# Kernel optimization log

Hardware: AMD Instinct MI355X
Metric: run time of the kernel (lower is better)

## Reference

```python
import jax, jax.numpy as jnp
import numpy as np

B, N, C = 64, 1700, 256
E_SP, E_TM = 6400, 10000


def gcn_conv(x, W, b, edge_index, num_nodes):
    """PyG GCNConv (normalize=True, add_self_loops=True) on batched [B,N,C] input,
    gathering/scattering along the node axis (node_dim=-2)."""
    row, col = edge_index[0], edge_index[1]
    loops = jnp.arange(num_nodes, dtype=row.dtype)
    row = jnp.concatenate([row, loops])
    col = jnp.concatenate([col, loops])
    w = jnp.ones(row.shape[0], dtype=x.dtype)
    deg = jax.ops.segment_sum(w, col, num_segments=num_nodes)
    dinv = jnp.where(deg > 0, jax.lax.rsqrt(deg), jnp.zeros_like(deg))
    norm = dinv[row] * dinv[col]                      # [E+N]
    h = x @ W                                         # [B,N,Cout]
    msg = h[:, row, :] * norm[None, :, None]          # gather along joints
    out = jnp.zeros((x.shape[0], num_nodes, W.shape[1]), x.dtype)
    out = out.at[:, col, :].add(msg)                  # scatter-add along joints
    return out + b


def setup_inputs() -> dict:
    key = jax.random.key(0)
    ks = jax.random.split(key, 9)
    s = 1.0 / np.sqrt(C)
    return {
        "x": jax.random.normal(ks[0], (B, N, C), jnp.float32),
        "W1": jax.random.uniform(ks[1], (C, C), jnp.float32, -s, s),
        "b1": jnp.zeros((C,), jnp.float32),
        "W2": jax.random.uniform(ks[2], (C, C), jnp.float32, -s, s),
        "b2": jnp.zeros((C,), jnp.float32),
        "W3": jax.random.uniform(ks[3], (C, C), jnp.float32, -s, s),
        "b3": jnp.zeros((C,), jnp.float32),
        "keypoint_line_without_temporal": jax.random.randint(ks[4], (2, E_SP), 0, N, jnp.int32),
        "keypoint_line_with_temporal": jax.random.randint(ks[5], (2, E_TM), 0, N, jnp.int32),
    }


def reference(x, W1, b1, W2, b2, W3, b3,
              keypoint_line_without_temporal, keypoint_line_with_temporal):
    num_nodes = x.shape[1]
    residual = x  # downsample is None -> identity residual
    out = jax.nn.relu(gcn_conv(x, W1, b1, keypoint_line_without_temporal, num_nodes))
    out = jax.nn.relu(gcn_conv(out, W2, b2, keypoint_line_with_temporal, num_nodes))
    out = gcn_conv(out, W3, b3, keypoint_line_without_temporal, num_nodes)
    return jax.nn.relu(out + residual)
```

## Files before the change

### kernel.cpp

```cpp
#include <hip/hip_runtime.h>

#define NNODES 1700
#define CDIM   256

typedef __attribute__((ext_vector_type(8))) short bf16x8;
typedef __attribute__((ext_vector_type(4))) float f32x4;

__device__ inline float bf2f(unsigned h) { return __uint_as_float(h << 16); }
__device__ inline unsigned short f2bf(float f) {
  unsigned u = __float_as_uint(f);
  u = (u + 0x7FFFu + ((u >> 16) & 1u)) >> 16;
  return (unsigned short)u;
}

__device__ inline void async_copy16(const void* gsrc, void* ldst) {
  __builtin_amdgcn_global_load_lds(
      (const __attribute__((address_space(1))) unsigned int*)gsrc,
      (__attribute__((address_space(3))) unsigned int*)ldst,
      16, 0, 0);
}


__global__ __launch_bounds__(256) void prep1(const float* __restrict__ W1,
                                             const float* __restrict__ W2,
                                             const float* __restrict__ W3,
                                             unsigned short* __restrict__ Wt,
                                             int* __restrict__ zb) {
  int i = blockIdx.x * 256 + threadIdx.x;
  if (i < 4 * NNODES) zb[i] = 0;
  if (i < 3 * 65536) {
    int wsel = i >> 16, e = i & 65535;
    const float* W = wsel == 0 ? W1 : (wsel == 1 ? W2 : W3);
    int k = e >> 8, n = e & 255;
    Wt[(wsel << 16) + n * 256 + k] = f2bf(W[e]);
  }
}

__global__ __launch_bounds__(256) void prep2(const int* __restrict__ esp, int Esp,
                                             const int* __restrict__ etm, int Etm,
                                             int* __restrict__ cnt_sp,
                                             int* __restrict__ cnt_tm) {
  int i = blockIdx.x * 256 + threadIdx.x;
  if (i < Esp) {
    atomicAdd(&cnt_sp[esp[Esp + i]], 1);
  } else {
    int k = i - Esp;
    if (k < Etm) atomicAdd(&cnt_tm[etm[Etm + k]], 1);
  }
}

__global__ __launch_bounds__(1024) void prep3(const int* __restrict__ cnt_sp,
                                              float* __restrict__ dinv_sp,
                                              int* __restrict__ off_sp,
                                              const int* __restrict__ cnt_tm,
                                              float* __restrict__ dinv_tm,
                                              int* __restrict__ off_tm) {
  const int* cnt = blockIdx.x ? cnt_tm : cnt_sp;
  float* dinv = blockIdx.x ? dinv_tm : dinv_sp;
  int* off = blockIdx.x ? off_tm : off_sp;
  __shared__ int s[2048];
  int t = threadIdx.x;
  for (int i = t; i < NNODES; i += 1024) dinv[i] = rsqrtf((float)(cnt[i] + 1));
  for (int i = t; i < 2048; i += 1024) s[i] = (i < NNODES) ? (cnt[i] + 1) : 0;
  for (int d = 1; d < 2048; d <<= 1) {
    __syncthreads();
    int idx = (t + 1) * (d << 1) - 1;
    if (idx < 2048) s[idx] += s[idx - d];
  }
  __syncthreads();
  if (t == 0) s[2047] = 0;
  for (int d = 1024; d >= 1; d >>= 1) {
    __syncthreads();
    int idx = (t + 1) * (d << 1) - 1;
    if (idx < 2048) { int tmp = s[idx - d]; s[idx - d] = s[idx]; s[idx] += tmp; }
  }
  __syncthreads();
  for (int i = t; i <= NNODES; i += 1024) off[i] = s[i];
}

__global__ __launch_bounds__(256) void prep4(
    const int* __restrict__ esp, int Esp, const int* __restrict__ etm, int Etm,
    const float* __restrict__ dinv_sp, const int* __restrict__ off_sp,
    int* __restrict__ cur_sp, int* __restrict__ src_sp, float* __restrict__ wgt_sp,
    const float* __restrict__ dinv_tm, const int* __restrict__ off_tm,
    int* __restrict__ cur_tm, int* __restrict__ src_tm, float* __restrict__ wgt_tm) {
  int i = blockIdx.x * 256 + threadIdx.x;
  const int tot_sp = Esp + NNODES;
  if (i < tot_sp) {
    int s, d;
    if (i < Esp) { s = esp[i]; d = esp[Esp + i]; } else { s = d = i - Esp; }
    float w = dinv_sp[s] * dinv_sp[d];
    int p = atomicAdd(&cur_sp[d], 1);
    int idx = off_sp[d] + p;
    src_sp[idx] = s; wgt_sp[idx] = w;
  } else {
    int k = i - tot_sp;
    if (k < Etm + NNODES) {
      int s, d;
      if (k < Etm) { s = etm[k]; d = etm[Etm + k]; } else { s = d = k - Etm; }
      float w = dinv_tm[s] * dinv_tm[d];
      int p = atomicAdd(&cur_tm[d], 1);
      int idx = off_tm[d] + p;
      src_tm[idx] = s; wgt_tm[idx] = w;
    }
  }
}


template <bool SRCF32>
__global__ __launch_bounds__(256) void agg_kernel(const void* __restrict__ Xp,
                                                  const int* __restrict__ off,
                                                  const int* __restrict__ srcv,
                                                  const float* __restrict__ wv,
                                                  unsigned short* __restrict__ Xa) {
  const int n = blockIdx.x;
  const int b = blockIdx.y * 8 + (threadIdx.x >> 5);
  const int c = (threadIdx.x & 31) * 8;
  const int beg = off[n], end = off[n + 1];
  const size_t base = (size_t)b * NNODES;

  float a0 = 0.f, a1 = 0.f, a2 = 0.f, a3 = 0.f;
  float a4 = 0.f, a5 = 0.f, a6 = 0.f, a7 = 0.f;
  for (int i = beg; i < end; i += 2) {
    int s0 = srcv[i];
    float w0 = wv[i];
    const bool two = (i + 1 < end);
    int i1 = two ? i + 1 : i;
    int s1 = srcv[i1];
    float w1 = two ? wv[i1] : 0.f;
    if (SRCF32) {
      const float* X = (const float*)Xp;
      const float* p0 = X + (base + s0) * CDIM + c;
      const float* p1 = X + (base + s1) * CDIM + c;
      float4 u0 = *(const float4*)p0, u1 = *(const float4*)(p0 + 4);
      float4 v0 = *(const float4*)p1, v1 = *(const float4*)(p1 + 4);
      a0 += w0 * u0.x + w1 * v0.x; a1 += w0 * u0.y + w1 * v0.y;
      a2 += w0 * u0.z + w1 * v0.z; a3 += w0 * u0.w + w1 * v0.w;
      a4 += w0 * u1.x + w1 * v1.x; a5 += w0 * u1.y + w1 * v1.y;
      a6 += w0 * u1.z + w1 * v1.z; a7 += w0 * u1.w + w1 * v1.w;
    } else {
      const unsigned short* X = (const unsigned short*)Xp;
      uint4 u = *(const uint4*)(X + (base + s0) * CDIM + c);
      uint4 v = *(const uint4*)(X + (base + s1) * CDIM + c);
      a0 += w0 * bf2f(u.x & 0xffffu) + w1 * bf2f(v.x & 0xffffu);
      a1 += w0 * bf2f(u.x >> 16)     + w1 * bf2f(v.x >> 16);
      a2 += w0 * bf2f(u.y & 0xffffu) + w1 * bf2f(v.y & 0xffffu);
      a3 += w0 * bf2f(u.y >> 16)     + w1 * bf2f(v.y >> 16);
      a4 += w0 * bf2f(u.z & 0xffffu) + w1 * bf2f(v.z & 0xffffu);
      a5 += w0 * bf2f(u.z >> 16)     + w1 * bf2f(v.z >> 16);
      a6 += w0 * bf2f(u.w & 0xffffu) + w1 * bf2f(v.w & 0xffffu);
      a7 += w0 * bf2f(u.w >> 16)     + w1 * bf2f(v.w >> 16);
    }
  }
  bf16x8 ov;
  ov[0] = (short)f2bf(a0); ov[1] = (short)f2bf(a1);
  ov[2] = (short)f2bf(a2); ov[3] = (short)f2bf(a3);
  ov[4] = (short)f2bf(a4); ov[5] = (short)f2bf(a5);
  ov[6] = (short)f2bf(a6); ov[7] = (short)f2bf(a7);
  *(bf16x8*)(Xa + (base + n) * CDIM + c) = ov;
}


template <int K>
__device__ __forceinline__ void kstep(const unsigned short* __restrict__ asrc,
                                      const unsigned short* __restrict__ bsrc,
                                      unsigned short (&As)[3][128 * 32],
                                      unsigned short (&Bs)[3][256 * 32],
                                      int t, int wm, int wn, int lr, int lk,
                                      f32x4 (&acc)[4][4]) {
  if constexpr (K < 7) {
    asm volatile("s_waitcnt vmcnt(3)" ::: "memory");
  } else {
    asm volatile("s_waitcnt vmcnt(0)" ::: "memory");
  }
  __builtin_amdgcn_s_barrier();
  if constexpr (K + 2 < 8) {
    constexpr int S = K + 2;
    async_copy16(asrc + S * 32, &As[S % 3][t * 8]);
    async_copy16(bsrc + S * 32, &Bs[S % 3][t * 8]);
    async_copy16(bsrc + 128 * CDIM + S * 32, &Bs[S % 3][4096 + t * 8]);
  }
  bf16x8 a[4], b[4];
#pragma unroll
  for (int i = 0; i < 4; i++)
    a[i] = *(const bf16x8*)&As[K % 3][(wm + i * 16 + lr) * 32 + lk];
#pragma unroll
  for (int i = 0; i < 4; i++)
    b[i] = *(const bf16x8*)&Bs[K % 3][(wn + i * 16 + lr) * 32 + lk];
#pragma unroll
  for (int mi = 0; mi < 4; mi++)
#pragma unroll
    for (int ni = 0; ni < 4; ni++)
      acc[mi][ni] = __builtin_amdgcn_mfma_f32_16x16x32_bf16(a[mi], b[ni], acc[mi][ni], 0, 0, 0);
}

template <bool FINAL>
__global__ __launch_bounds__(512, 4) void gemm_n256(const unsigned short* __restrict__ A,
                                                    const unsigned short* __restrict__ Wt,
                                                    const float* __restrict__ bias,
                                                    const float* __restrict__ resid,
                                                    void* __restrict__ outp) {
  __shared__ __align__(16) unsigned short As[3][128 * 32];
  __shared__ __align__(16) unsigned short Bs[3][256 * 32];
  const int m0 = blockIdx.x * 128;
  const int t = threadIdx.x;
  const int lane = t & 63;
  const int w = t >> 6;
  const int wm = (w & 1) * 64;
  const int wn = (w >> 1) * 64;
  const int lr = lane & 15;
  const int lk = (lane >> 4) * 8;

  const unsigned short* asrc = A + (size_t)(m0 + (t >> 2)) * CDIM + (t & 3) * 8;
  const unsigned short* bsrc = Wt + (size_t)(t >> 2) * CDIM + (t & 3) * 8;

  f32x4 acc[4][4] = {};

#pragma unroll
  for (int s = 0; s < 2; s++) {
    async_copy16(asrc + s * 32, &As[s][t * 8]);
    async_copy16(bsrc + s * 32, &Bs[s][t * 8]);
    async_copy16(bsrc + 128 * CDIM + s * 32, &Bs[s][4096 + t * 8]);
  }

  kstep<0>(asrc, bsrc, As, Bs, t, wm, wn, lr, lk, acc);
  kstep<1>(asrc, bsrc, As, Bs, t, wm, wn, lr, lk, acc);
  kstep<2>(asrc, bsrc, As, Bs, t, wm, wn, lr, lk, acc);
  kstep<3>(asrc, bsrc, As, Bs, t, wm, wn, lr, lk, acc);
  kstep<4>(asrc, bsrc, As, Bs, t, wm, wn, lr, lk, acc);
  kstep<5>(asrc, bsrc, As, Bs, t, wm, wn, lr, lk, acc);
  kstep<6>(asrc, bsrc, As, Bs, t, wm, wn, lr, lk, acc);
  kstep<7>(asrc, bsrc, As, Bs, t, wm, wn, lr, lk, acc);

  float bv[4];
#pragma unroll
  for (int ni = 0; ni < 4; ni++) bv[ni] = bias[wn + ni * 16 + lr];
  const int orow = (lane >> 4) * 4;
#pragma unroll
  for (int mi = 0; mi < 4; mi++) {
#pragma unroll
    for (int ni = 0; ni < 4; ni++) {
#pragma unroll
      for (int r = 0; r < 4; r++) {
        const size_t gr = (size_t)(m0 + wm + mi * 16 + orow + r);
        const size_t idx = gr * CDIM + wn + ni * 16 + lr;
        float v = acc[mi][ni][r] + bv[ni];
        if (FINAL) {
          v += resid[idx];
          ((float*)outp)[idx] = fmaxf(v, 0.f);
        } else {
          ((unsigned short*)outp)[idx] = f2bf(fmaxf(v, 0.f));
        }
      }
    }
  }
}


extern "C" void kernel_launch(void* const* d_in, const int* in_sizes, int n_in,
                              void* d_out, int out_size, void* d_ws, size_t ws_size,
                              hipStream_t stream) {
  const float* x  = (const float*)d_in[0];
  const float* W1 = (const float*)d_in[1];
  const float* b1 = (const float*)d_in[2];
  const float* W2 = (const float*)d_in[3];
  const float* b2 = (const float*)d_in[4];
  const float* W3 = (const float*)d_in[5];
  const float* b3 = (const float*)d_in[6];
  const int* esp = (const int*)d_in[7];
  const int* etm = (const int*)d_in[8];

  const int Esp = in_sizes[7] / 2;
  const int Etm = in_sizes[8] / 2;
  const int B = in_sizes[0] / (NNODES * CDIM);
  const int M = B * NNODES;

  char* ws = (char*)d_ws;
  size_t woff = 0;
  auto alloc = [&](size_t bytes) -> void* {
    void* p = ws + woff;
    woff = (woff + bytes + 255) & ~(size_t)255;
    return p;
  };

  unsigned short* H   = (unsigned short*)alloc((size_t)M * CDIM * 2);
  unsigned short* Act = (unsigned short*)alloc((size_t)M * CDIM * 2);
  unsigned short* Wt  = (unsigned short*)alloc((size_t)3 * CDIM * CDIM * 2);
  int* zero_base = (int*)alloc((size_t)4 * NNODES * sizeof(int));
  int* cnt_sp = zero_base;
  int* cur_sp = zero_base + NNODES;
  int* cnt_tm = zero_base + 2 * NNODES;
  int* cur_tm = zero_base + 3 * NNODES;
  int* off_sp = (int*)alloc((NNODES + 1) * sizeof(int));
  int* off_tm = (int*)alloc((NNODES + 1) * sizeof(int));
  float* dinv_sp = (float*)alloc(NNODES * sizeof(float));
  float* dinv_tm = (float*)alloc(NNODES * sizeof(float));
  int*   src_sp = (int*)alloc((size_t)(Esp + NNODES) * sizeof(int));
  float* wgt_sp = (float*)alloc((size_t)(Esp + NNODES) * sizeof(float));
  int*   src_tm = (int*)alloc((size_t)(Etm + NNODES) * sizeof(int));
  float* wgt_tm = (float*)alloc((size_t)(Etm + NNODES) * sizeof(float));

  prep1<<<(3 * 65536 + 255) / 256, 256, 0, stream>>>(W1, W2, W3, Wt, zero_base);
  prep2<<<(Esp + Etm + 255) / 256, 256, 0, stream>>>(esp, Esp, etm, Etm, cnt_sp, cnt_tm);
  prep3<<<2, 1024, 0, stream>>>(cnt_sp, dinv_sp, off_sp, cnt_tm, dinv_tm, off_tm);
  prep4<<<(Esp + Etm + 2 * NNODES + 255) / 256, 256, 0, stream>>>(
      esp, Esp, etm, Etm, dinv_sp, off_sp, cur_sp, src_sp, wgt_sp,
      dinv_tm, off_tm, cur_tm, src_tm, wgt_tm);

  dim3 agrid(NNODES, B / 8);
  dim3 ggrid(M / 128);

  agg_kernel<true><<<agrid, 256, 0, stream>>>(x, off_sp, src_sp, wgt_sp, Act);
  gemm_n256<false><<<ggrid, 512, 0, stream>>>(Act, Wt, b1, nullptr, H);
  agg_kernel<false><<<agrid, 256, 0, stream>>>(H, off_tm, src_tm, wgt_tm, Act);
  gemm_n256<false><<<ggrid, 512, 0, stream>>>(Act, Wt + CDIM * CDIM, b2, nullptr, H);
  agg_kernel<false><<<agrid, 256, 0, stream>>>(H, off_sp, src_sp, wgt_sp, Act);
  gemm_n256<true><<<ggrid, 512, 0, stream>>>(Act, Wt + 2 * CDIM * CDIM, b3, x, d_out);
}
```

Before: 465.9 us.

## Split GEMM into 128x64 tiles with swizzled block order and double buffering

The GEMM no longer computes one 128x256 output tile per 512-thread block. It now launches four times as many 256-thread blocks, each producing a 128x64 tile. Blocks are remapped with a chunked swizzle so neighbouring blocks share A rows in cache. The LDS pipeline drops from a triple buffer to a double buffer, with an extra barrier after fragment reads so the next prefetch can safely overwrite the buffer. The goal is more blocks for occupancy and load balance on the 256 CUs, at the cost of reading each A tile four times and adding a barrier per k-step.

```diff
diff --git a/kernel.cpp b/kernel.cpp
--- a/kernel.cpp
+++ b/kernel.cpp
@@ -164,63 +164,70 @@
 template <int K>
 __device__ __forceinline__ void kstep(const unsigned short* __restrict__ asrc,
                                       const unsigned short* __restrict__ bsrc,
-                                      unsigned short (&As)[3][128 * 32],
-                                      unsigned short (&Bs)[3][256 * 32],
+                                      unsigned short (&As)[2][128 * 32],
+                                      unsigned short (&Bs)[2][64 * 32],
                                       int t, int wm, int wn, int lr, int lk,
-                                      f32x4 (&acc)[4][4]) {
+                                      f32x4 (&acc)[4][2]) {
   if constexpr (K < 7) {
     asm volatile("s_waitcnt vmcnt(3)" ::: "memory");
   } else {
     asm volatile("s_waitcnt vmcnt(0)" ::: "memory");
   }
   __builtin_amdgcn_s_barrier();
+  bf16x8 a[4], b[2];
+#pragma unroll
+  for (int i = 0; i < 4; i++)
+    a[i] = *(const bf16x8*)&As[K & 1][(wm + i * 16 + lr) * 32 + lk];
+#pragma unroll
+  for (int i = 0; i < 2; i++)
+    b[i] = *(const bf16x8*)&Bs[K & 1][(wn + i * 16 + lr) * 32 + lk];
+  asm volatile("s_waitcnt lgkmcnt(0)" ::: "memory");
+  __builtin_amdgcn_sched_barrier(0);
+  __builtin_amdgcn_s_barrier();
   if constexpr (K + 2 < 8) {
     constexpr int S = K + 2;
-    async_copy16(asrc + S * 32, &As[S % 3][t * 8]);
-    async_copy16(bsrc + S * 32, &Bs[S % 3][t * 8]);
-    async_copy16(bsrc + 128 * CDIM + S * 32, &Bs[S % 3][4096 + t * 8]);
-  }
-  bf16x8 a[4], b[4];
-#pragma unroll
-  for (int i = 0; i < 4; i++)
-    a[i] = *(const bf16x8*)&As[K % 3][(wm + i * 16 + lr) * 32 + lk];
-#pragma unroll
-  for (int i = 0; i < 4; i++)
-    b[i] = *(const bf16x8*)&Bs[K % 3][(wn + i * 16 + lr) * 32 + lk];
+    async_copy16(asrc + S * 32, &As[S & 1][t * 8]);
+    async_copy16(asrc + (size_t)64 * CDIM + S * 32, &As[S & 1][2048 + t * 8]);
+    async_copy16(bsrc + S * 32, &Bs[S & 1][t * 8]);
+  }
 #pragma unroll
   for (int mi = 0; mi < 4; mi++)
 #pragma unroll
-    for (int ni = 0; ni < 4; ni++)
+    for (int ni = 0; ni < 2; ni++)
       acc[mi][ni] = __builtin_amdgcn_mfma_f32_16x16x32_bf16(a[mi], b[ni], acc[mi][ni], 0, 0, 0);
 }
 
 template <bool FINAL>
-__global__ __launch_bounds__(512, 4) void gemm_n256(const unsigned short* __restrict__ A,
-                                                    const unsigned short* __restrict__ Wt,
-                                                    const float* __restrict__ bias,
-                                                    const float* __restrict__ resid,
-                                                    void* __restrict__ outp) {
-  __shared__ __align__(16) unsigned short As[3][128 * 32];
-  __shared__ __align__(16) unsigned short Bs[3][256 * 32];
-  const int m0 = blockIdx.x * 128;
+__global__ __launch_bounds__(256, 5) void gemm_t64(const unsigned short* __restrict__ A,
+                                                   const unsigned short* __restrict__ Wt,
+                                                   const float* __restrict__ bias,
+                                                   const float* __restrict__ resid,
+                                                   void* __restrict__ outp) {
+  __shared__ __align__(16) unsigned short As[2][128 * 32];
+  __shared__ __align__(16) unsigned short Bs[2][64 * 32];
   const int t = threadIdx.x;
   const int lane = t & 63;
   const int w = t >> 6;
   const int wm = (w & 1) * 64;
-  const int wn = (w >> 1) * 64;
+  const int wn = (w >> 1) * 32;
   const int lr = lane & 15;
   const int lk = (lane >> 4) * 8;
 
+  const int chunk = gridDim.x >> 3;
+  const int swz = (blockIdx.x & 7) * chunk + (blockIdx.x >> 3);
+  const int m0 = (swz >> 2) * 128;
+  const int n0 = (swz & 3) * 64;
+
   const unsigned short* asrc = A + (size_t)(m0 + (t >> 2)) * CDIM + (t & 3) * 8;
-  const unsigned short* bsrc = Wt + (size_t)(t >> 2) * CDIM + (t & 3) * 8;
-
-  f32x4 acc[4][4] = {};
+  const unsigned short* bsrc = Wt + (size_t)(n0 + (t >> 2)) * CDIM + (t & 3) * 8;
+
+  f32x4 acc[4][2] = {};
 
 #pragma unroll
   for (int s = 0; s < 2; s++) {
     async_copy16(asrc + s * 32, &As[s][t * 8]);
+    async_copy16(asrc + (size_t)64 * CDIM + s * 32, &As[s][2048 + t * 8]);
     async_copy16(bsrc + s * 32, &Bs[s][t * 8]);
-    async_copy16(bsrc + 128 * CDIM + s * 32, &Bs[s][4096 + t * 8]);
   }
 
   kstep<0>(asrc, bsrc, As, Bs, t, wm, wn, lr, lk, acc);
@@ -232,18 +239,18 @@
   kstep<6>(asrc, bsrc, As, Bs, t, wm, wn, lr, lk, acc);
   kstep<7>(asrc, bsrc, As, Bs, t, wm, wn, lr, lk, acc);
 
-  float bv[4];
-#pragma unroll
-  for (int ni = 0; ni < 4; ni++) bv[ni] = bias[wn + ni * 16 + lr];
+  float bv[2];
+#pragma unroll
+  for (int ni = 0; ni < 2; ni++) bv[ni] = bias[n0 + wn + ni * 16 + lr];
   const int orow = (lane >> 4) * 4;
 #pragma unroll
   for (int mi = 0; mi < 4; mi++) {
 #pragma unroll
-    for (int ni = 0; ni < 4; ni++) {
+    for (int ni = 0; ni < 2; ni++) {
 #pragma unroll
       for (int r = 0; r < 4; r++) {
         const size_t gr = (size_t)(m0 + wm + mi * 16 + orow + r);
-        const size_t idx = gr * CDIM + wn + ni * 16 + lr;
+        const size_t idx = gr * CDIM + n0 + wn + ni * 16 + lr;
         float v = acc[mi][ni][r] + bv[ni];
         if (FINAL) {
           v += resid[idx];
@@ -308,12 +315,12 @@
       dinv_tm, off_tm, cur_tm, src_tm, wgt_tm);
 
   dim3 agrid(NNODES, B / 8);
-  dim3 ggrid(M / 128);
+  dim3 ggrid(4 * (M / 128));
 
   agg_kernel<true><<<agrid, 256, 0, stream>>>(x, off_sp, src_sp, wgt_sp, Act);
-  gemm_n256<false><<<ggrid, 512, 0, stream>>>(Act, Wt, b1, nullptr, H);
+  gemm_t64<false><<<ggrid, 256, 0, stream>>>(Act, Wt, b1, nullptr, H);
   agg_kernel<false><<<agrid, 256, 0, stream>>>(H, off_tm, src_tm, wgt_tm, Act);
-  gemm_n256<false><<<ggrid, 512, 0, stream>>>(Act, Wt + CDIM * CDIM, b2, nullptr, H);
+  gemm_t64<false><<<ggrid, 256, 0, stream>>>(Act, Wt + CDIM * CDIM, b2, nullptr, H);
   agg_kernel<false><<<agrid, 256, 0, stream>>>(H, off_sp, src_sp, wgt_sp, Act);
-  gemm_n256<true><<<ggrid, 512, 0, stream>>>(Act, Wt + 2 * CDIM * CDIM, b3, x, d_out);
-}
+  gemm_t64<true><<<ggrid, 256, 0, stream>>>(Act, Wt + 2 * CDIM * CDIM, b3, x, d_out);
+}
```

Result: faster. 437.5 us (-6.1%).

## Remap aggregation blocks per XCD and stream GEMM operands directly from global

Applied to the files above, without the earlier changes.

The aggregation grid becomes 1D and is remapped so that each XCD handles a contiguous range of (batch, node-group) tiles, and each block covers 8 nodes of one batch, so gathered rows of one batch stay in that XCD's L2. The LDS-staged 128x256 GEMM with async copies is replaced by a register-only kernel where each wave computes a 16x128 tile, loading A fragments and weight fragments straight from global memory. This removes LDS traffic and barriers but relies on L2 and cache for weight reuse, and issues many more small global loads per wave.

```diff
diff --git a/kernel.cpp b/kernel.cpp
--- a/kernel.cpp
+++ b/kernel.cpp
@@ -11,13 +11,6 @@
   unsigned u = __float_as_uint(f);
   u = (u + 0x7FFFu + ((u >> 16) & 1u)) >> 16;
   return (unsigned short)u;
-}
-
-__device__ inline void async_copy16(const void* gsrc, void* ldst) {
-  __builtin_amdgcn_global_load_lds(
-      (const __attribute__((address_space(1))) unsigned int*)gsrc,
-      (__attribute__((address_space(3))) unsigned int*)ldst,
-      16, 0, 0);
 }
 
 
@@ -113,8 +106,12 @@
                                                   const int* __restrict__ srcv,
                                                   const float* __restrict__ wv,
                                                   unsigned short* __restrict__ Xa) {
-  const int n = blockIdx.x;
-  const int b = blockIdx.y * 8 + (threadIdx.x >> 5);
+  const int xcd = blockIdx.x & 7, pos = blockIdx.x >> 3;
+  const int l = xcd * 1704 + pos;
+  const int b = l / 213;
+  const int ngrp = l - b * 213;
+  const int n = ngrp * 8 + (threadIdx.x >> 5);
+  if (n >= NNODES) return;
   const int c = (threadIdx.x & 31) * 8;
   const int beg = off[n], end = off[n + 1];
   const size_t base = (size_t)b * NNODES;
@@ -161,96 +158,55 @@
 }
 
 
-template <int K>
-__device__ __forceinline__ void kstep(const unsigned short* __restrict__ asrc,
-                                      const unsigned short* __restrict__ bsrc,
-                                      unsigned short (&As)[3][128 * 32],
-                                      unsigned short (&Bs)[3][256 * 32],
-                                      int t, int wm, int wn, int lr, int lk,
-                                      f32x4 (&acc)[4][4]) {
-  if constexpr (K < 7) {
-    asm volatile("s_waitcnt vmcnt(3)" ::: "memory");
-  } else {
-    asm volatile("s_waitcnt vmcnt(0)" ::: "memory");
-  }
-  __builtin_amdgcn_s_barrier();
-  if constexpr (K + 2 < 8) {
-    constexpr int S = K + 2;
-    async_copy16(asrc + S * 32, &As[S % 3][t * 8]);
-    async_copy16(bsrc + S * 32, &Bs[S % 3][t * 8]);
-    async_copy16(bsrc + 128 * CDIM + S * 32, &Bs[S % 3][4096 + t * 8]);
-  }
-  bf16x8 a[4], b[4];
-#pragma unroll
-  for (int i = 0; i < 4; i++)
-    a[i] = *(const bf16x8*)&As[K % 3][(wm + i * 16 + lr) * 32 + lk];
-#pragma unroll
-  for (int i = 0; i < 4; i++)
-    b[i] = *(const bf16x8*)&Bs[K % 3][(wn + i * 16 + lr) * 32 + lk];
-#pragma unroll
-  for (int mi = 0; mi < 4; mi++)
-#pragma unroll
-    for (int ni = 0; ni < 4; ni++)
-      acc[mi][ni] = __builtin_amdgcn_mfma_f32_16x16x32_bf16(a[mi], b[ni], acc[mi][ni], 0, 0, 0);
-}
-
 template <bool FINAL>
-__global__ __launch_bounds__(512, 4) void gemm_n256(const unsigned short* __restrict__ A,
-                                                    const unsigned short* __restrict__ Wt,
-                                                    const float* __restrict__ bias,
-                                                    const float* __restrict__ resid,
-                                                    void* __restrict__ outp) {
-  __shared__ __align__(16) unsigned short As[3][128 * 32];
-  __shared__ __align__(16) unsigned short Bs[3][256 * 32];
-  const int m0 = blockIdx.x * 128;
+__global__ __launch_bounds__(256, 4) void gemm_stream(const unsigned short* __restrict__ A,
+                                                      const unsigned short* __restrict__ Wt,
+                                                      const float* __restrict__ bias,
+                                                      const float* __restrict__ resid,
+                                                      void* __restrict__ outp) {
   const int t = threadIdx.x;
   const int lane = t & 63;
   const int w = t >> 6;
-  const int wm = (w & 1) * 64;
-  const int wn = (w >> 1) * 64;
   const int lr = lane & 15;
   const int lk = (lane >> 4) * 8;
 
-  const unsigned short* asrc = A + (size_t)(m0 + (t >> 2)) * CDIM + (t & 3) * 8;
-  const unsigned short* bsrc = Wt + (size_t)(t >> 2) * CDIM + (t & 3) * 8;
-
-  f32x4 acc[4][4] = {};
-
-#pragma unroll
-  for (int s = 0; s < 2; s++) {
-    async_copy16(asrc + s * 32, &As[s][t * 8]);
-    async_copy16(bsrc + s * 32, &Bs[s][t * 8]);
-    async_copy16(bsrc + 128 * CDIM + s * 32, &Bs[s][4096 + t * 8]);
-  }
-
-  kstep<0>(asrc, bsrc, As, Bs, t, wm, wn, lr, lk, acc);
-  kstep<1>(asrc, bsrc, As, Bs, t, wm, wn, lr, lk, acc);
-  kstep<2>(asrc, bsrc, As, Bs, t, wm, wn, lr, lk, acc);
-  kstep<3>(asrc, bsrc, As, Bs, t, wm, wn, lr, lk, acc);
-  kstep<4>(asrc, bsrc, As, Bs, t, wm, wn, lr, lk, acc);
-  kstep<5>(asrc, bsrc, As, Bs, t, wm, wn, lr, lk, acc);
-  kstep<6>(asrc, bsrc, As, Bs, t, wm, wn, lr, lk, acc);
-  kstep<7>(asrc, bsrc, As, Bs, t, wm, wn, lr, lk, acc);
-
-  float bv[4];
-#pragma unroll
-  for (int ni = 0; ni < 4; ni++) bv[ni] = bias[wn + ni * 16 + lr];
+  const int rt = blockIdx.x * 2 + (w >> 1);
+  const int nb = (w & 1) * 128;
+  const int m0 = rt * 16;
+
+  const unsigned short* arow = A + (size_t)(m0 + lr) * CDIM + lk;
+  const unsigned short* brow = Wt + (size_t)(nb + lr) * CDIM + lk;
+
+  bf16x8 a[8];
+#pragma unroll
+  for (int kc = 0; kc < 8; kc++)
+    a[kc] = *(const bf16x8*)(arow + kc * 32);
+
+  f32x4 acc[8] = {};
+#pragma unroll
+  for (int kc = 0; kc < 8; kc++) {
+    bf16x8 b[8];
+#pragma unroll
+    for (int ni = 0; ni < 8; ni++)
+      b[ni] = *(const bf16x8*)(brow + (size_t)ni * 16 * CDIM + kc * 32);
+#pragma unroll
+    for (int ni = 0; ni < 8; ni++)
+      acc[ni] = __builtin_amdgcn_mfma_f32_16x16x32_bf16(a[kc], b[ni], acc[ni], 0, 0, 0);
+  }
+
   const int orow = (lane >> 4) * 4;
 #pragma unroll
-  for (int mi = 0; mi < 4; mi++) {
-#pragma unroll
-    for (int ni = 0; ni < 4; ni++) {
-#pragma unroll
-      for (int r = 0; r < 4; r++) {
-        const size_t gr = (size_t)(m0 + wm + mi * 16 + orow + r);
-        const size_t idx = gr * CDIM + wn + ni * 16 + lr;
-        float v = acc[mi][ni][r] + bv[ni];
-        if (FINAL) {
-          v += resid[idx];
-          ((float*)outp)[idx] = fmaxf(v, 0.f);
-        } else {
-          ((unsigned short*)outp)[idx] = f2bf(fmaxf(v, 0.f));
-        }
+  for (int ni = 0; ni < 8; ni++) {
+    const float bv = bias[nb + ni * 16 + lr];
+#pragma unroll
+    for (int r = 0; r < 4; r++) {
+      const size_t idx = (size_t)(m0 + orow + r) * CDIM + nb + ni * 16 + lr;
+      float v = acc[ni][r] + bv;
+      if (FINAL) {
+        v += resid[idx];
+        ((float*)outp)[idx] = fmaxf(v, 0.f);
+      } else {
+        ((unsigned short*)outp)[idx] = f2bf(fmaxf(v, 0.f));
       }
     }
   }
@@ -307,13 +263,13 @@
       esp, Esp, etm, Etm, dinv_sp, off_sp, cur_sp, src_sp, wgt_sp,
       dinv_tm, off_tm, cur_tm, src_tm, wgt_tm);
 
-  dim3 agrid(NNODES, B / 8);
-  dim3 ggrid(M / 128);
+  dim3 agrid(213 * 64);
+  dim3 ggrid(M / 32);
 
   agg_kernel<true><<<agrid, 256, 0, stream>>>(x, off_sp, src_sp, wgt_sp, Act);
-  gemm_n256<false><<<ggrid, 512, 0, stream>>>(Act, Wt, b1, nullptr, H);
+  gemm_stream<false><<<ggrid, 256, 0, stream>>>(Act, Wt, b1, nullptr, H);
   agg_kernel<false><<<agrid, 256, 0, stream>>>(H, off_tm, src_tm, wgt_tm, Act);
-  gemm_n256<false><<<ggrid, 512, 0, stream>>>(Act, Wt + CDIM * CDIM, b2, nullptr, H);
+  gemm_stream<false><<<ggrid, 256, 0, stream>>>(Act, Wt + CDIM * CDIM, b2, nullptr, H);
   agg_kernel<false><<<agrid, 256, 0, stream>>>(H, off_sp, src_sp, wgt_sp, Act);
-  gemm_n256<true><<<ggrid, 512, 0, stream>>>(Act, Wt + 2 * CDIM * CDIM, b3, x, d_out);
-}
+  gemm_stream<true><<<ggrid, 256, 0, stream>>>(Act, Wt + 2 * CDIM * CDIM, b3, x, d_out);
+}
```

Result: slower. 658.5 us (+41.3%).
